# Optimization experiments

Measured on AMD Instinct MI355X. Metric: run time of the kernel, lower is better.

Reference implementation:

```python
import jax, jax.numpy as jnp
import numpy as np

B, T, U, V = 8, 200, 50, 1024
BLANK = 0


def setup_inputs() -> dict:
    key = jax.random.key(0)
    k1, k2, k3, k4 = jax.random.split(key, 4)
    h = jax.random.normal(k1, (B, T, U, V), dtype=jnp.float32)
    # target label ids (never blank), one per non-blank token slot
    targets = jax.random.randint(k2, (B, U - 1), 1, V)
    # valid lengths in [T//2, T] and [U//2, U]
    input_lens = jax.random.randint(k3, (B,), T // 2, T + 1)
    target_lens = jax.random.randint(k4, (B,), U // 2, U + 1)
    return {"h": h, "targets": targets, "input_lens": input_lens, "target_lens": target_lens}


def _rnnt_neg_log_probs(h, targets, input_lens, target_lens):
    # NOTE: faithful to source: LogSoftmax over dim=1 (the frame axis), as written.
    logp = jax.nn.log_softmax(h, axis=1)          # (B,T,U,V)
    blank = logp[..., BLANK]                      # (B,T,U)
    # emit[b,t,u] = logp[b,t,u, targets[b,u]] for u in 0..U-2
    emit = jnp.take_along_axis(logp[:, :, : U - 1, :], targets[:, None, :, None], axis=3)[..., 0]  # (B,T,U-1)

    # row t=0: log_alpha[0,u] = sum_{k<u} emit[:,0,k]
    row0 = jnp.concatenate([jnp.zeros((B, 1), logp.dtype), jnp.cumsum(emit[:, 0, :], axis=1)], axis=1)  # (B,U)

    def outer(prev_row, xs):
        blank_t, emit_t = xs                      # blank[:,t-1,:] (B,U), emit[:,t,:] (B,U-1)
        a = prev_row + blank_t                    # vertical (blank) path, (B,U)
        c0 = a[:, 0]                              # u == 0 entry

        def inner(c, x):
            au, em = x                            # each (B,)
            new = jnp.logaddexp(au, c + em)
            return new, new

        _, rest = jax.lax.scan(inner, c0, (a[:, 1:].T, emit_t.T))  # (U-1,B)
        new_row = jnp.concatenate([c0[:, None], rest.T], axis=1)   # (B,U)
        return new_row, new_row

    xs = (jnp.swapaxes(blank[:, : T - 1, :], 0, 1),   # (T-1,B,U)
          jnp.swapaxes(emit[:, 1:, :], 0, 1))         # (T-1,B,U-1)
    _, rows = jax.lax.scan(outer, row0, xs)            # (T-1,B,U)
    log_alpha = jnp.concatenate([row0[None], rows], axis=0).transpose(1, 0, 2)  # (B,T,U)

    bidx = jnp.arange(B)
    ti = input_lens - 1
    ui = target_lens - 1
    final = log_alpha[bidx, ti, ui] + blank[bidx, ti, ui]
    return -final                                  # (B,)


def reference(h, targets, input_lens, target_lens):
    return jnp.mean(_rnnt_neg_log_probs(h, targets, input_lens, target_lens))
```

## Files before the change

### kernel.cpp

```cpp
#include <hip/hip_runtime.h>
#include <math.h>

#define B 8
#define T 200
#define U 50
#define V 1024

__device__ __forceinline__ float wave_max(float v) {
    #pragma unroll
    for (int off = 32; off > 0; off >>= 1)
        v = fmaxf(v, __shfl_xor(v, off, 64));
    return v;
}
__device__ __forceinline__ float wave_sum(float v) {
    #pragma unroll
    for (int off = 32; off > 0; off >>= 1)
        v += __shfl_xor(v, off, 64);
    return v;
}

__global__ void lse_kernel(const float* __restrict__ h,
                           const int* __restrict__ targets,
                           float* __restrict__ blank_ws,
                           float* __restrict__ emit_ws,
                           float* __restrict__ out) {
    const int u = blockIdx.x;
    const int b = blockIdx.y;
    const int which = blockIdx.z;
    const int lane = threadIdx.x;

    if (u == 0 && b == 0 && which == 0 && lane == 0) out[0] = 0.f;
    if (which == 1 && u >= U - 1) return;

    const int v = (which == 0) ? 0 : targets[b * (U - 1) + u];
    const float* base = h + (size_t)b * T * U * V + (size_t)u * V + v;

    float x[4];
    float m = -INFINITY;
    #pragma unroll
    for (int k = 0; k < 4; ++k) {
        const int t = lane + 64 * k;
        x[k] = (t < T) ? base[(size_t)t * U * V] : -INFINITY;
        m = fmaxf(m, x[k]);
    }
    m = wave_max(m);
    float s = 0.f;
    #pragma unroll
    for (int k = 0; k < 4; ++k)
        s += __expf(x[k] - m);
    s = wave_sum(s);
    const float lse = m + __logf(s);

    float* outp = (which == 0)
        ? blank_ws + ((size_t)b * U + u) * T
        : emit_ws + ((size_t)b * (U - 1) + u) * T;
    #pragma unroll
    for (int k = 0; k < 4; ++k) {
        const int t = lane + 64 * k;
        if (t < T) outp[t] = x[k] - lse;
    }
}

__global__ __launch_bounds__(512)
void dp_kernel(const float* __restrict__ blank_ws,
               const float* __restrict__ emit_ws,
               const int* __restrict__ input_lens,
               const int* __restrict__ target_lens,
               float* __restrict__ out) {
    __shared__ float s_all[U * T + (U - 1) * T];

    const int b = blockIdx.x;
    const int tid = threadIdx.x;
    const int ti = input_lens[b] - 1;
    const int ui = target_lens[b] - 1;

    {
        const float4* gb = (const float4*)(blank_ws + (size_t)b * U * T);
        const float4* ge = (const float4*)(emit_ws + (size_t)b * (U - 1) * T);
        float4* s4 = (float4*)s_all;
        constexpr int NB = (U * T) / 4;
        constexpr int NT = (U * T + (U - 1) * T) / 4;
        for (int i = tid; i < NT; i += 512)
            s4[i] = (i < NB) ? gb[i] : ge[i - NB];
    }
    __syncthreads();

    if (tid >= 64) return;
    const float* s_bl = s_all;
    const float* s_em = s_all + U * T;

    const int u = tid;
    const int uc = (u < U) ? u : (U - 1);
    const int ue = (u >= 1) ? ((u <= U - 1) ? u - 1 : U - 2) : 0;
    const float* bl_row = s_bl + uc * T;
    const float* em_row = s_em + ue * T;

    const int dmax = ti + ui;
    float a_prev = (u == 0) ? 0.f : -INFINITY;
    float result = (dmax == 0 && u == 0) ? 0.f : -INFINITY;

    auto clampT = [](int x) { return x < 0 ? 0 : (x > T - 1 ? T - 1 : x); };

    float bl_c = bl_row[clampT(0 - u)];
    float em_c = em_row[clampT(1 - u)];

    for (int d = 1; d <= dmax; ++d) {
        const float left = __shfl_up(a_prev, 1, 64);
        const float bl_n = bl_row[clampT(d - u)];
        const float em_n = em_row[clampT(d + 1 - u)];
        const int t = d - u;
        const bool cell = (t >= 0) && (t < T) && (u < U);
        const float term1 = (cell && t >= 1) ? a_prev + bl_c : -INFINITY;
        const float term2 = (cell && u >= 1) ? left + em_c : -INFINITY;
        const float mx = fmaxf(term1, term2);
        const float a_new = (mx == -INFINITY)
            ? -INFINITY
            : mx + __logf(1.f + __expf(fminf(term1, term2) - mx));
        if (cell) a_prev = a_new;
        if (d == dmax && u == ui) result = a_new;
        bl_c = bl_n;
        em_c = em_n;
    }
    if (u == ui)
        atomicAdd(out, -(result + s_bl[ui * T + ti]) * (1.f / (float)B));
}

extern "C" void kernel_launch(void* const* d_in, const int* in_sizes, int n_in,
                              void* d_out, int out_size, void* d_ws, size_t ws_size,
                              hipStream_t stream) {
    const float* h = (const float*)d_in[0];
    const int* targets = (const int*)d_in[1];
    const int* input_lens = (const int*)d_in[2];
    const int* target_lens = (const int*)d_in[3];
    float* out = (float*)d_out;

    float* blank_ws = (float*)d_ws;
    float* emit_ws = blank_ws + (size_t)B * U * T;

    dim3 g1(U, B, 2);
    lse_kernel<<<g1, 64, 0, stream>>>(h, targets, blank_ws, emit_ws, out);
    dp_kernel<<<B, 512, 0, stream>>>(blank_ws, emit_ws, input_lens, target_lens, out);
}
```

Baseline: 397.3 us.

## Fuse log-softmax gather into DP kernel per batch, finalize with partials

Merges the log-softmax column kernel into the DP kernel so each batch block computes the blank and emit log-probabilities directly into shared memory, skipping the global workspace round trip. The atomic accumulation is replaced by per-batch partials plus a tiny finalize kernel. The trade-off is that the gather phase now runs on only 8 blocks of 1024 threads instead of 800 small blocks. That cuts the parallelism available to hide the latency of strided global loads.

```diff
diff --git a/kernel.cpp b/kernel.cpp
--- a/kernel.cpp
+++ b/kernel.cpp
@@ -5,6 +5,7 @@
 #define T 200
 #define U 50
 #define V 1024
+#define NCOL (2 * U - 1)
 
 __device__ __forceinline__ float wave_max(float v) {
     #pragma unroll
@@ -19,69 +20,45 @@
     return v;
 }
 
-__global__ void lse_kernel(const float* __restrict__ h,
-                           const int* __restrict__ targets,
-                           float* __restrict__ blank_ws,
-                           float* __restrict__ emit_ws,
-                           float* __restrict__ out) {
-    const int u = blockIdx.x;
-    const int b = blockIdx.y;
-    const int which = blockIdx.z;
-    const int lane = threadIdx.x;
-
-    if (u == 0 && b == 0 && which == 0 && lane == 0) out[0] = 0.f;
-    if (which == 1 && u >= U - 1) return;
-
-    const int v = (which == 0) ? 0 : targets[b * (U - 1) + u];
-    const float* base = h + (size_t)b * T * U * V + (size_t)u * V + v;
-
-    float x[4];
-    float m = -INFINITY;
-    #pragma unroll
-    for (int k = 0; k < 4; ++k) {
-        const int t = lane + 64 * k;
-        x[k] = (t < T) ? base[(size_t)t * U * V] : -INFINITY;
-        m = fmaxf(m, x[k]);
-    }
-    m = wave_max(m);
-    float s = 0.f;
-    #pragma unroll
-    for (int k = 0; k < 4; ++k)
-        s += __expf(x[k] - m);
-    s = wave_sum(s);
-    const float lse = m + __logf(s);
-
-    float* outp = (which == 0)
-        ? blank_ws + ((size_t)b * U + u) * T
-        : emit_ws + ((size_t)b * (U - 1) + u) * T;
-    #pragma unroll
-    for (int k = 0; k < 4; ++k) {
-        const int t = lane + 64 * k;
-        if (t < T) outp[t] = x[k] - lse;
-    }
-}
-
-__global__ __launch_bounds__(512)
-void dp_kernel(const float* __restrict__ blank_ws,
-               const float* __restrict__ emit_ws,
-               const int* __restrict__ input_lens,
-               const int* __restrict__ target_lens,
-               float* __restrict__ out) {
-    __shared__ float s_all[U * T + (U - 1) * T];
-
+__global__ __launch_bounds__(1024)
+void rnnt_fused(const float* __restrict__ h,
+                const int* __restrict__ targets,
+                const int* __restrict__ input_lens,
+                const int* __restrict__ target_lens,
+                float* __restrict__ partials) {
+    __shared__ float s_all[NCOL * T];
     const int b = blockIdx.x;
     const int tid = threadIdx.x;
-    const int ti = input_lens[b] - 1;
-    const int ui = target_lens[b] - 1;
+    const int wv = tid >> 6;
+    const int lane = tid & 63;
 
-    {
-        const float4* gb = (const float4*)(blank_ws + (size_t)b * U * T);
-        const float4* ge = (const float4*)(emit_ws + (size_t)b * (U - 1) * T);
-        float4* s4 = (float4*)s_all;
-        constexpr int NB = (U * T) / 4;
-        constexpr int NT = (U * T + (U - 1) * T) / 4;
-        for (int i = tid; i < NT; i += 512)
-            s4[i] = (i < NB) ? gb[i] : ge[i - NB];
+    for (int c = wv; c < NCOL; c += 16) {
+        const int u = (c >= U) ? c - U : c;
+        const int v = (c >= U) ? targets[b * (U - 1) + u] : 0;
+        const float* base = h + (size_t)b * T * U * V + (size_t)u * V + v;
+
+        float x[4];
+        float m = -INFINITY;
+        #pragma unroll
+        for (int k = 0; k < 4; ++k) {
+            const int t = lane + 64 * k;
+            x[k] = (t < T) ? base[(size_t)t * U * V] : -INFINITY;
+            m = fmaxf(m, x[k]);
+        }
+        m = wave_max(m);
+        float s = 0.f;
+        #pragma unroll
+        for (int k = 0; k < 4; ++k)
+            s += __expf(x[k] - m);
+        s = wave_sum(s);
+        const float lse = m + __logf(s);
+
+        float* dst = s_all + c * T;
+        #pragma unroll
+        for (int k = 0; k < 4; ++k) {
+            const int t = lane + 64 * k;
+            if (t < T) dst[t] = x[k] - lse;
+        }
     }
     __syncthreads();
 
@@ -90,6 +67,9 @@
     const float* s_em = s_all + U * T;
 
     const int u = tid;
+    const int ti = input_lens[b] - 1;
+    const int ui = target_lens[b] - 1;
+
     const int uc = (u < U) ? u : (U - 1);
     const int ue = (u >= 1) ? ((u <= U - 1) ? u - 1 : U - 2) : 0;
     const float* bl_row = s_bl + uc * T;
@@ -122,7 +102,14 @@
         em_c = em_n;
     }
     if (u == ui)
-        atomicAdd(out, -(result + s_bl[ui * T + ti]) * (1.f / (float)B));
+        partials[b] = -(result + s_bl[ui * T + ti]);
+}
+
+__global__ void finalize_kernel(const float* __restrict__ partials,
+                                float* __restrict__ out) {
+    float s = (threadIdx.x < B) ? partials[threadIdx.x] : 0.f;
+    s = wave_sum(s);
+    if (threadIdx.x == 0) out[0] = s * (1.f / (float)B);
 }
 
 extern "C" void kernel_launch(void* const* d_in, const int* in_sizes, int n_in,
@@ -133,11 +120,8 @@
     const int* input_lens = (const int*)d_in[2];
     const int* target_lens = (const int*)d_in[3];
     float* out = (float*)d_out;
+    float* partials = (float*)d_ws;
 
-    float* blank_ws = (float*)d_ws;
-    float* emit_ws = blank_ws + (size_t)B * U * T;
-
-    dim3 g1(U, B, 2);
-    lse_kernel<<<g1, 64, 0, stream>>>(h, targets, blank_ws, emit_ws, out);
-    dp_kernel<<<B, 512, 0, stream>>>(blank_ws, emit_ws, input_lens, target_lens, out);
+    rnnt_fused<<<B, 1024, 0, stream>>>(h, targets, input_lens, target_lens, partials);
+    finalize_kernel<<<1, 64, 0, stream>>>(partials, out);
 }
```

New measurement: 427.8 us. 7.7% more time.
